# Kernel optimization log

Measured on AMD Instinct MI355X. Metric: run time of the kernel, lower is better.

## Reference

```python
import jax, jax.numpy as jnp
import numpy as np

N = 16  # lpcoeffs_N, LPC order


def setup_inputs() -> dict:
    key = jax.random.key(0)
    # [B, T, N] LPC coefficients; small magnitude keeps (1 - ki^2) well-conditioned
    x = (jax.random.uniform(key, (64, 32768, N), dtype=jnp.float32) - 0.5) * 0.2
    return {"x": x}


def reference(x):
    # Levinson step-down: LPC -> reflection coefficients (RC).
    # At step i, split into leading j-1 coeffs `a` and already-finalized tail `b`.
    # ki is the current reflection coefficient (first element of the tail).
    for i in range(1, N):
        j = N - i + 1
        a = x[:, :, : j - 1]          # [B, T, j-1]
        b = x[:, :, j - 1 :]          # [B, T, N-j+1]
        ki = b[:, :, 0:1]             # [B, T, 1], broadcasts over last axis
        temp = (a - ki * a[:, :, ::-1]) / (1.0 - ki * ki)
        x = jnp.concatenate([temp, b], axis=2)  # [B, T, N]
    return x
```

## Files before the change

kernel.cpp:

```cpp
#include <hip/hip_runtime.h>


constexpr int N = 16;
constexpr int RS = 17;
constexpr int WAVES_PER_WG = 4;

typedef float f32x4 __attribute__((ext_vector_type(4)));

__global__ __launch_bounds__(256) void lpc2rc_kernel(const float* __restrict__ x,
                                                     float* __restrict__ out,
                                                     int nrows) {
    __shared__ float lds[WAVES_PER_WG * 64 * RS];

    const int tid  = threadIdx.x;
    const int wave = tid >> 6;
    const int lane = tid & 63;
    float* __restrict__ wlds = lds + wave * 64 * RS;

    const long long wave_row0 = ((long long)blockIdx.x * WAVES_PER_WG + wave) * 64;

    float a[N];

    if (wave_row0 + 64 <= (long long)nrows) {
        const f32x4* __restrict__ in4 = (const f32x4*)x;
        f32x4* __restrict__ out4 = (f32x4*)out;
        const long long base4 = wave_row0 * 4;

        f32x4 ld[4];
#pragma unroll
        for (int c = 0; c < 4; ++c)
            ld[c] = in4[base4 + (long long)(c * 64 + lane)];

#pragma unroll
        for (int c = 0; c < 4; ++c) {
            float* p = wlds + (16 * c + (lane >> 2)) * RS + 4 * (lane & 3);
            p[0] = ld[c].x; p[1] = ld[c].y; p[2] = ld[c].z; p[3] = ld[c].w;
        }

        {
            const float* p = wlds + lane * RS;
#pragma unroll
            for (int e = 0; e < N; ++e) a[e] = p[e];
        }

        float inv_s = 1.0f;
#pragma unroll
        for (int i = 1; i < N; ++i) {
            const int len = N - i;
            const float k = a[len] * inv_s;
            a[len] = k;
            const float r = __builtin_amdgcn_rcpf(1.0f - k * k);
            inv_s *= r;
#pragma unroll
            for (int m = 0; m < len / 2; ++m) {
                const int j = len - 1 - m;
                const float am = a[m];
                const float aj = a[j];
                a[m] = __builtin_fmaf(-k, aj, am);
                a[j] = __builtin_fmaf(-k, am, aj);
            }
            if (len & 1) {
                const int mid = len / 2;
                const float t = a[mid];
                a[mid] = __builtin_fmaf(-k, t, t);
            }
        }
        a[0] *= inv_s;

        {
            float* p = wlds + lane * RS;
#pragma unroll
            for (int e = 0; e < N; ++e) p[e] = a[e];
        }

#pragma unroll
        for (int c = 0; c < 4; ++c) {
            const float* p = wlds + (16 * c + (lane >> 2)) * RS + 4 * (lane & 3);
            f32x4 v;
            v.x = p[0]; v.y = p[1]; v.z = p[2]; v.w = p[3];
            __builtin_nontemporal_store(v, &out4[base4 + (long long)(c * 64 + lane)]);
        }
    } else {
        const long long r = wave_row0 + lane;
        if (r >= (long long)nrows) return;
        const f32x4* __restrict__ in4 = (const f32x4*)x;
        f32x4* __restrict__ out4 = (f32x4*)out;
        f32x4 v0 = in4[r * 4 + 0], v1 = in4[r * 4 + 1],
              v2 = in4[r * 4 + 2], v3 = in4[r * 4 + 3];
        a[0]=v0.x; a[1]=v0.y; a[2]=v0.z; a[3]=v0.w;
        a[4]=v1.x; a[5]=v1.y; a[6]=v1.z; a[7]=v1.w;
        a[8]=v2.x; a[9]=v2.y; a[10]=v2.z; a[11]=v2.w;
        a[12]=v3.x; a[13]=v3.y; a[14]=v3.z; a[15]=v3.w;

        float inv_s = 1.0f;
#pragma unroll
        for (int i = 1; i < N; ++i) {
            const int len = N - i;
            const float k = a[len] * inv_s;
            a[len] = k;
            const float rr = __builtin_amdgcn_rcpf(1.0f - k * k);
            inv_s *= rr;
#pragma unroll
            for (int m = 0; m < len / 2; ++m) {
                const int j = len - 1 - m;
                const float am = a[m], aj = a[j];
                a[m] = __builtin_fmaf(-k, aj, am);
                a[j] = __builtin_fmaf(-k, am, aj);
            }
            if (len & 1) {
                const int mid = len / 2;
                const float t = a[mid];
                a[mid] = __builtin_fmaf(-k, t, t);
            }
        }
        a[0] *= inv_s;

        v0.x=a[0]; v0.y=a[1]; v0.z=a[2]; v0.w=a[3];
        v1.x=a[4]; v1.y=a[5]; v1.z=a[6]; v1.w=a[7];
        v2.x=a[8]; v2.y=a[9]; v2.z=a[10]; v2.w=a[11];
        v3.x=a[12]; v3.y=a[13]; v3.z=a[14]; v3.w=a[15];
        __builtin_nontemporal_store(v0, &out4[r * 4 + 0]);
        __builtin_nontemporal_store(v1, &out4[r * 4 + 1]);
        __builtin_nontemporal_store(v2, &out4[r * 4 + 2]);
        __builtin_nontemporal_store(v3, &out4[r * 4 + 3]);
    }
}

extern "C" void kernel_launch(void* const* d_in, const int* in_sizes, int n_in,
                              void* d_out, int out_size, void* d_ws, size_t ws_size,
                              hipStream_t stream) {
    const float* x = (const float*)d_in[0];
    float* out = (float*)d_out;
    const int nrows = in_sizes[0] / N;
    const int rows_per_wg = 64 * WAVES_PER_WG;
    const int grid = (nrows + rows_per_wg - 1) / rows_per_wg;
    lpc2rc_kernel<<<grid, 256, 0, stream>>>(x, out, nrows);
}
```

Baseline: 230.0 us.

## Replace LDS transpose with in-register DPP quad transpose

Removes the shared-memory staging used to give each lane a full 16-coefficient row. Loaded float4 chunks are instead transposed within each quad using DPP xor-1 and xor-2 lane swaps plus selects, so each lane ends up holding a whole (permuted) row, and the inverse permutation restores the layout before the store. This avoids LDS writes, reads and the LDS allocation, but adds many DPP moves and selects. It also switches nontemporal stores to regular stores and adds a minimum-occupancy hint to launch bounds.

```diff
diff --git a/kernel.cpp b/kernel.cpp
--- a/kernel.cpp
+++ b/kernel.cpp
@@ -2,22 +2,26 @@
 
 
 constexpr int N = 16;
-constexpr int RS = 17;
 constexpr int WAVES_PER_WG = 4;
 
 typedef float f32x4 __attribute__((ext_vector_type(4)));
 
-__global__ __launch_bounds__(256) void lpc2rc_kernel(const float* __restrict__ x,
-                                                     float* __restrict__ out,
-                                                     int nrows) {
-    __shared__ float lds[WAVES_PER_WG * 64 * RS];
+__device__ __forceinline__ float dpp_xor2(float x) {
+    const int xi = __float_as_int(x);
+    return __int_as_float(__builtin_amdgcn_update_dpp(xi, xi, 0x4E, 0xF, 0xF, true));
+}
+__device__ __forceinline__ float dpp_xor1(float x) {
+    const int xi = __float_as_int(x);
+    return __int_as_float(__builtin_amdgcn_update_dpp(xi, xi, 0xB1, 0xF, 0xF, true));
+}
 
+__global__ __launch_bounds__(256, 8) void lpc2rc_kernel(const float* __restrict__ x,
+                                                        float* __restrict__ out,
+                                                        int nrows) {
     const int tid  = threadIdx.x;
-    const int wave = tid >> 6;
     const int lane = tid & 63;
-    float* __restrict__ wlds = lds + wave * 64 * RS;
 
-    const long long wave_row0 = ((long long)blockIdx.x * WAVES_PER_WG + wave) * 64;
+    const long long wave_row0 = ((long long)blockIdx.x * WAVES_PER_WG + (tid >> 6)) * 64;
 
     float a[N];
 
@@ -31,16 +35,31 @@
         for (int c = 0; c < 4; ++c)
             ld[c] = in4[base4 + (long long)(c * 64 + lane)];
 
+        const bool hi = (lane >> 1) & 1;
+        const bool lo = lane & 1;
+
+        float W[4][4];
 #pragma unroll
-        for (int c = 0; c < 4; ++c) {
-            float* p = wlds + (16 * c + (lane >> 2)) * RS + 4 * (lane & 3);
-            p[0] = ld[c].x; p[1] = ld[c].y; p[2] = ld[c].z; p[3] = ld[c].w;
+        for (int t = 0; t < 4; ++t) {
+            const float x0 = dpp_xor2(ld[0][t]);
+            const float x1 = dpp_xor2(ld[1][t]);
+            const float x2 = dpp_xor2(ld[2][t]);
+            const float x3 = dpp_xor2(ld[3][t]);
+            W[0][t] = hi ? x2 : ld[0][t];
+            W[1][t] = hi ? x3 : ld[1][t];
+            W[2][t] = hi ? ld[2][t] : x0;
+            W[3][t] = hi ? ld[3][t] : x1;
         }
-
-        {
-            const float* p = wlds + lane * RS;
 #pragma unroll
-            for (int e = 0; e < N; ++e) a[e] = p[e];
+        for (int t = 0; t < 4; ++t) {
+            const float y0 = dpp_xor1(W[0][t]);
+            const float y1 = dpp_xor1(W[1][t]);
+            const float y2 = dpp_xor1(W[2][t]);
+            const float y3 = dpp_xor1(W[3][t]);
+            a[0  + t] = lo ? y1 : W[0][t];
+            a[4  + t] = lo ? W[1][t] : y0;
+            a[8  + t] = lo ? y3 : W[2][t];
+            a[12 + t] = lo ? W[3][t] : y2;
         }
 
         float inv_s = 1.0f;
@@ -67,19 +86,33 @@
         }
         a[0] *= inv_s;
 
-        {
-            float* p = wlds + lane * RS;
 #pragma unroll
-            for (int e = 0; e < N; ++e) p[e] = a[e];
+        for (int t = 0; t < 4; ++t) {
+            const float x0 = dpp_xor2(a[0  + t]);
+            const float x1 = dpp_xor2(a[4  + t]);
+            const float x2 = dpp_xor2(a[8  + t]);
+            const float x3 = dpp_xor2(a[12 + t]);
+            W[0][t] = hi ? x2 : a[0  + t];
+            W[1][t] = hi ? x3 : a[4  + t];
+            W[2][t] = hi ? a[8  + t] : x0;
+            W[3][t] = hi ? a[12 + t] : x1;
+        }
+        f32x4 st[4];
+#pragma unroll
+        for (int t = 0; t < 4; ++t) {
+            const float y0 = dpp_xor1(W[0][t]);
+            const float y1 = dpp_xor1(W[1][t]);
+            const float y2 = dpp_xor1(W[2][t]);
+            const float y3 = dpp_xor1(W[3][t]);
+            st[0][t] = lo ? y1 : W[0][t];
+            st[1][t] = lo ? W[1][t] : y0;
+            st[2][t] = lo ? y3 : W[2][t];
+            st[3][t] = lo ? W[3][t] : y2;
         }
 
 #pragma unroll
-        for (int c = 0; c < 4; ++c) {
-            const float* p = wlds + (16 * c + (lane >> 2)) * RS + 4 * (lane & 3);
-            f32x4 v;
-            v.x = p[0]; v.y = p[1]; v.z = p[2]; v.w = p[3];
-            __builtin_nontemporal_store(v, &out4[base4 + (long long)(c * 64 + lane)]);
-        }
+        for (int c = 0; c < 4; ++c)
+            out4[base4 + (long long)(c * 64 + lane)] = st[c];
     } else {
         const long long r = wave_row0 + lane;
         if (r >= (long long)nrows) return;
@@ -119,10 +152,8 @@
         v1.x=a[4]; v1.y=a[5]; v1.z=a[6]; v1.w=a[7];
         v2.x=a[8]; v2.y=a[9]; v2.z=a[10]; v2.w=a[11];
         v3.x=a[12]; v3.y=a[13]; v3.z=a[14]; v3.w=a[15];
-        __builtin_nontemporal_store(v0, &out4[r * 4 + 0]);
-        __builtin_nontemporal_store(v1, &out4[r * 4 + 1]);
-        __builtin_nontemporal_store(v2, &out4[r * 4 + 2]);
-        __builtin_nontemporal_store(v3, &out4[r * 4 + 3]);
+        out4[r * 4 + 0] = v0; out4[r * 4 + 1] = v1;
+        out4[r * 4 + 2] = v2; out4[r * 4 + 3] = v3;
     }
 }
 
```

Result: no change. 227.6 us (-1.1%).
